# Optimization experiments

Hardware: AMD Instinct MI355X
Metric: run time of the kernel (lower is better)

Reference implementation:

```python
import jax, jax.numpy as jnp
import numpy as np


def setup_inputs() -> dict:
    key = jax.random.key(0)
    k1, k2, k3 = jax.random.split(key, 3)
    num, c_in, c_out, nx, ny, din, dout = 128, 3, 8, 31, 31, 4, 6
    x = jax.random.normal(k1, (num, c_in, din, nx + 1, ny + 1), dtype=jnp.float32)
    tensors = jax.random.normal(k2, (c_in, c_out, nx, ny, din, din, din, din, dout), dtype=jnp.float32)
    bias = jax.random.normal(k3, (c_out, nx, ny, dout), dtype=jnp.float32) * 1e-8
    return {"x": x, "tensors": tensors, "bias": bias}


def reference(x, tensors, bias):
    # x: [num, c_in, din, sx, sy]; tensors: [c_in, c_out, nx, ny, din,din,din,din, dout]
    num, c_in, din, sx, sy = x.shape
    X, Y = sx - 1, sy - 1  # == nx, ny
    c_out, dout = tensors.shape[1], tensors.shape[-1]
    # four 2x2-patch corners, each [num, c_in, din, X, Y]
    a = x[:, :, :, :-1, :-1]
    b = x[:, :, :, 1:, :-1]
    c = x[:, :, :, :-1, 1:]
    d = x[:, :, :, 1:, 1:]
    # outer product of the four corner vectors -> rank-4 local feature [num, c_in, din^4, X, Y]
    ab = jnp.einsum('ncixy,ncjxy->ncijxy', a, b)
    cd = jnp.einsum('nckxy,nclxy->ncklxy', c, d)
    patch = jnp.einsum('ncijxy,ncklxy->ncijklxy', ab, cd)
    patch = patch.reshape(num, c_in, din ** 4, X, Y)
    # per-position weight: [c_in, c_out, X, Y, din^4, dout]
    w = tensors.reshape(c_in, c_out, X, Y, din ** 4, dout)
    out = jnp.einsum('ncmxy,cpxymo->npoxy', patch, w)  # [num, c_out, dout, X, Y]
    out = out + bias.transpose(0, 3, 1, 2)[None]  # bias -> [1, c_out, dout, X, Y]
    return out
```

## Files before the change

kernel.cpp:

```cpp
#include <hip/hip_runtime.h>
#include <hip/hip_bf16.h>


typedef __attribute__((ext_vector_type(8))) short short8;
typedef __attribute__((ext_vector_type(4))) float floatx4;

#define WS_ELEMS (961u * 6144u)
#define SW_STR 72

static __device__ __forceinline__ unsigned pkbf(float lo, float hi) {
  __hip_bfloat162 h = __float22bfloat162_rn(make_float2(lo, hi));
  union { __hip_bfloat162 h; unsigned u; } v;
  v.h = h;
  return v.u;
}

template <bool TO_WS>
__global__ __launch_bounds__(256, 4)
void ttn_conv_mfma(const float* __restrict__ x,
                   const float* __restrict__ tensors,
                   const float* __restrict__ bias,
                   float* __restrict__ dst) {
  __shared__ __align__(16) unsigned short sW[2][48 * SW_STR];

  const int site = blockIdx.x;
  const int xx = site / 31, yy = site - xx * 31;
  const int t = threadIdx.x;
  const int lane = t & 63, wave = t >> 6;
  const int row = lane & 15, quad = lane >> 4;

  const int p_st = t >> 5, q_st = t & 31;

  floatx4 acc[2][3];
#pragma unroll
  for (int i0 = 0; i0 < 2; ++i0)
#pragma unroll
    for (int j0 = 0; j0 < 3; ++j0)
      acc[i0][j0] = (floatx4){0.f, 0.f, 0.f, 0.f};

  float a4[2][4], b2[2][2], cd8[2][8];
  float4 wv0, wv1, wv2;

  auto loadW = [&](int c, int mb) {
    const float* src = tensors +
        ((size_t)((c * 8 + p_st) * 961 + site)) * 1536 + (size_t)(mb * 64 + 2 * q_st) * 6;
    wv0 = *(const float4*)src;
    wv1 = *(const float4*)(src + 4);
    wv2 = *(const float4*)(src + 8);
  };
  auto storeW = [&](int buf) {
    const float vv[12] = {wv0.x, wv0.y, wv0.z, wv0.w, wv1.x, wv1.y,
                          wv1.z, wv1.w, wv2.x, wv2.y, wv2.z, wv2.w};
#pragma unroll
    for (int o = 0; o < 6; ++o)
      *(unsigned*)&sW[buf][(p_st * 6 + o) * SW_STR + 2 * q_st] = pkbf(vv[o], vv[o + 6]);
  };
  auto loadFactors = [&](int c) {
#pragma unroll
    for (int mt = 0; mt < 2; ++mt) {
      const int n = wave * 32 + mt * 16 + row;
      const float* xb = x + ((size_t)n * 3 + c) * 4096 + xx * 32 + yy;
      float dq[4];
#pragma unroll
      for (int i = 0; i < 4; ++i) {
        a4[mt][i] = xb[i * 1024];
        dq[i]     = xb[i * 1024 + 33];
      }
      b2[mt][0] = xb[(quad >> 1) * 1024 + 32];
      b2[mt][1] = xb[(2 + (quad >> 1)) * 1024 + 32];
      const float cq0 = xb[(2 * (quad & 1)) * 1024 + 1];
      const float cq1 = xb[(2 * (quad & 1) + 1) * 1024 + 1];
#pragma unroll
      for (int j = 0; j < 8; ++j)
        cd8[mt][j] = (j < 4 ? cq0 : cq1) * dq[j & 3];
    }
  };

  loadW(0, 0);
  storeW(0);
  loadW(0, 1);
  loadFactors(0);

  for (int c = 0; c < 3; ++c) {
    if (c) loadFactors(c);
#pragma unroll
    for (int mb = 0; mb < 4; ++mb) {
      const int ch = c * 4 + mb;
      const int bp = mb & 1;
      __syncthreads();

#pragma unroll
      for (int ks = 0; ks < 2; ++ks) {
        short8 bfr[3];
#pragma unroll
        for (int nt = 0; nt < 3; ++nt)
          bfr[nt] = *(const short8*)&sW[bp][(nt * 16 + row) * SW_STR + ks * 32 + quad * 8];
#pragma unroll
        for (int mt = 0; mt < 2; ++mt) {
          const float ab = a4[mt][mb] * b2[mt][ks];
          union { unsigned u[4]; short8 s; } af;
#pragma unroll
          for (int jj = 0; jj < 4; ++jj)
            af.u[jj] = pkbf(ab * cd8[mt][2 * jj], ab * cd8[mt][2 * jj + 1]);
#pragma unroll
          for (int nt = 0; nt < 3; ++nt)
            acc[mt][nt] = __builtin_amdgcn_mfma_f32_16x16x32_bf16(
                af.s, bfr[nt], acc[mt][nt], 0, 0, 0);
        }
      }

      if (ch < 11) storeW(1 - bp);
      if (ch < 10) {
        const int i2 = ch + 2;
        loadW(i2 >> 2, i2 & 3);
      }
    }
  }

  if (TO_WS) {
#pragma unroll
    for (int mt = 0; mt < 2; ++mt)
#pragma unroll
      for (int r = 0; r < 4; ++r) {
        const int n = wave * 32 + mt * 16 + quad * 4 + r;
#pragma unroll
        for (int nt = 0; nt < 3; ++nt) {
          const int po = nt * 16 + row;
          dst[(size_t)site * 6144 + n * 48 + po] = acc[mt][nt][r];
        }
      }
  } else {
#pragma unroll
    for (int mt = 0; mt < 2; ++mt)
#pragma unroll
      for (int r = 0; r < 4; ++r) {
        const int n = wave * 32 + mt * 16 + quad * 4 + r;
#pragma unroll
        for (int nt = 0; nt < 3; ++nt) {
          const int po = nt * 16 + row;
          const int p = po / 6, o = po - p * 6;
          dst[(size_t)(n * 48 + po) * 961 + site] =
              acc[mt][nt][r] + bias[(p * 961 + site) * 6 + o];
        }
      }
  }
}

__global__ __launch_bounds__(256, 8)
void ttn_transpose_bias(const float* __restrict__ ws,
                        const float* __restrict__ bias,
                        float* __restrict__ out) {
  __shared__ float tile[32][33];
  const int f0 = blockIdx.x * 32;
  const int s0 = blockIdx.y * 32;
  const int tx = threadIdx.x;
  const int ty = threadIdx.y;

#pragma unroll
  for (int rr = 0; rr < 4; ++rr) {
    const int srow = ty + rr * 8;
    const int site = s0 + srow;
    if (site < 961)
      tile[srow][tx] = ws[(size_t)site * 6144 + f0 + tx];
  }
  __syncthreads();

#pragma unroll
  for (int rr = 0; rr < 4; ++rr) {
    const int fy = ty + rr * 8;
    const int f = f0 + fy;
    const int site = s0 + tx;
    if (site < 961) {
      const int po = f % 48;
      const int p = po / 6, o = po - p * 6;
      out[(size_t)f * 961 + site] = tile[tx][fy] + bias[(p * 961 + site) * 6 + o];
    }
  }
}

extern "C" void kernel_launch(void* const* d_in, const int* in_sizes, int n_in,
                              void* d_out, int out_size, void* d_ws, size_t ws_size,
                              hipStream_t stream) {
  const float* x       = (const float*)d_in[0];
  const float* tensors = (const float*)d_in[1];
  const float* bias    = (const float*)d_in[2];
  float* out           = (float*)d_out;

  const size_t need = (size_t)WS_ELEMS * sizeof(float);
  if (d_ws != nullptr && ws_size >= need) {
    float* ws = (float*)d_ws;
    hipLaunchKernelGGL((ttn_conv_mfma<true>), dim3(961), dim3(256), 0, stream,
                       x, tensors, bias, ws);
    hipLaunchKernelGGL(ttn_transpose_bias, dim3(192, 31), dim3(32, 8), 0, stream,
                       ws, bias, out);
  } else {
    hipLaunchKernelGGL((ttn_conv_mfma<false>), dim3(961), dim3(256), 0, stream,
                       x, tensors, bias, out);
  }
}
```

Baseline: 255.4 us.

## Process two weight chunks per barrier stage and prefetch raw x factors early

The shared-memory weight tile is widened so each double-buffered stage holds two 64-column chunks. That halves the number of __syncthreads across the 12 chunks, and the store and next global load now happen before each stage's MFMAs. The x corner values are fetched with float2 loads one stage ahead of when they are turned into a/b/cd factors, hiding their global latency behind MFMA work. The cost is more live registers (twice the weight prefetch registers plus raw x buffers) under a 4-blocks-per-CU launch bound, which risks spills or lower occupancy. Both a larger LDS footprint and unaligned float2 loads are possible side costs.

```diff
diff --git a/kernel.cpp b/kernel.cpp
--- a/kernel.cpp
+++ b/kernel.cpp
@@ -6,7 +6,7 @@
 typedef __attribute__((ext_vector_type(4))) float floatx4;
 
 #define WS_ELEMS (961u * 6144u)
-#define SW_STR 72
+#define SW_COLS 136
 
 static __device__ __forceinline__ unsigned pkbf(float lo, float hi) {
   __hip_bfloat162 h = __float22bfloat162_rn(make_float2(lo, hi));
@@ -21,7 +21,7 @@
                    const float* __restrict__ tensors,
                    const float* __restrict__ bias,
                    float* __restrict__ dst) {
-  __shared__ __align__(16) unsigned short sW[2][48 * SW_STR];
+  __shared__ __align__(16) unsigned short sW[2][48 * SW_COLS];
 
   const int site = blockIdx.x;
   const int xx = site / 31, yy = site - xx * 31;
@@ -39,82 +39,97 @@
       acc[i0][j0] = (floatx4){0.f, 0.f, 0.f, 0.f};
 
   float a4[2][4], b2[2][2], cd8[2][8];
-  float4 wv0, wv1, wv2;
-
-  auto loadW = [&](int c, int mb) {
-    const float* src = tensors +
-        ((size_t)((c * 8 + p_st) * 961 + site)) * 1536 + (size_t)(mb * 64 + 2 * q_st) * 6;
-    wv0 = *(const float4*)src;
-    wv1 = *(const float4*)(src + 4);
-    wv2 = *(const float4*)(src + 8);
-  };
-  auto storeW = [&](int buf) {
-    const float vv[12] = {wv0.x, wv0.y, wv0.z, wv0.w, wv1.x, wv1.y,
-                          wv1.z, wv1.w, wv2.x, wv2.y, wv2.z, wv2.w};
-#pragma unroll
-    for (int o = 0; o < 6; ++o)
-      *(unsigned*)&sW[buf][(p_st * 6 + o) * SW_STR + 2 * q_st] = pkbf(vv[o], vv[o + 6]);
-  };
-  auto loadFactors = [&](int c) {
+  float2 rAC[2][4], rBD[2][4];
+  float4 wv[6];
+
+  auto loadPair = [&](int s) {
+    const int c = s >> 1;
+    const float* base = tensors + ((size_t)((c * 8 + p_st) * 961 + site)) * 1536;
+#pragma unroll
+    for (int h = 0; h < 2; ++h) {
+      const float* src = base + (size_t)((2 * (s & 1) + h) * 64 + 2 * q_st) * 6;
+      wv[h * 3 + 0] = *(const float4*)src;
+      wv[h * 3 + 1] = *(const float4*)(src + 4);
+      wv[h * 3 + 2] = *(const float4*)(src + 8);
+    }
+  };
+  auto storePair = [&](int buf) {
+#pragma unroll
+    for (int h = 0; h < 2; ++h) {
+      const float4 w0 = wv[h * 3], w1 = wv[h * 3 + 1], w2 = wv[h * 3 + 2];
+      const float vv[12] = {w0.x, w0.y, w0.z, w0.w, w1.x, w1.y,
+                            w1.z, w1.w, w2.x, w2.y, w2.z, w2.w};
+#pragma unroll
+      for (int o = 0; o < 6; ++o)
+        *(unsigned*)&sW[buf][(p_st * 6 + o) * SW_COLS + h * 64 + 2 * q_st] =
+            pkbf(vv[o], vv[o + 6]);
+    }
+  };
+  auto loadRaw = [&](int c) {
 #pragma unroll
     for (int mt = 0; mt < 2; ++mt) {
       const int n = wave * 32 + mt * 16 + row;
       const float* xb = x + ((size_t)n * 3 + c) * 4096 + xx * 32 + yy;
-      float dq[4];
 #pragma unroll
       for (int i = 0; i < 4; ++i) {
-        a4[mt][i] = xb[i * 1024];
-        dq[i]     = xb[i * 1024 + 33];
-      }
-      b2[mt][0] = xb[(quad >> 1) * 1024 + 32];
-      b2[mt][1] = xb[(2 + (quad >> 1)) * 1024 + 32];
-      const float cq0 = xb[(2 * (quad & 1)) * 1024 + 1];
-      const float cq1 = xb[(2 * (quad & 1) + 1) * 1024 + 1];
+        rAC[mt][i] = *(const float2*)(xb + i * 1024);
+        rBD[mt][i] = *(const float2*)(xb + i * 1024 + 32);
+      }
+    }
+  };
+  auto cvtFactors = [&]() {
+    const int qh = quad >> 1, ql = quad & 1;
+#pragma unroll
+    for (int mt = 0; mt < 2; ++mt) {
+#pragma unroll
+      for (int i = 0; i < 4; ++i) a4[mt][i] = rAC[mt][i].x;
+      b2[mt][0] = qh ? rBD[mt][1].x : rBD[mt][0].x;
+      b2[mt][1] = qh ? rBD[mt][3].x : rBD[mt][2].x;
+      const float cq0 = ql ? rAC[mt][2].y : rAC[mt][0].y;
+      const float cq1 = ql ? rAC[mt][3].y : rAC[mt][1].y;
 #pragma unroll
       for (int j = 0; j < 8; ++j)
-        cd8[mt][j] = (j < 4 ? cq0 : cq1) * dq[j & 3];
-    }
-  };
-
-  loadW(0, 0);
-  storeW(0);
-  loadW(0, 1);
-  loadFactors(0);
-
-  for (int c = 0; c < 3; ++c) {
-    if (c) loadFactors(c);
-#pragma unroll
-    for (int mb = 0; mb < 4; ++mb) {
-      const int ch = c * 4 + mb;
-      const int bp = mb & 1;
-      __syncthreads();
-
-#pragma unroll
-      for (int ks = 0; ks < 2; ++ks) {
-        short8 bfr[3];
+        cd8[mt][j] = (j < 4 ? cq0 : cq1) * rBD[mt][j & 3].y;
+    }
+  };
+
+  loadPair(0);
+  loadRaw(0);
+  cvtFactors();
+  storePair(0);
+  loadPair(1);
+  __syncthreads();
+
+#pragma unroll
+  for (int s = 0; s < 6; ++s) {
+    const int bp = s & 1;
+    if (s <= 4) storePair(1 - bp);
+    if (s <= 3) loadPair(s + 2);
+    if (s == 1) loadRaw(1);
+    if (s == 3) loadRaw(2);
+    if (s == 2 || s == 4) cvtFactors();
+
+#pragma unroll
+    for (int ks = 0; ks < 4; ++ks) {
+      const int mb = 2 * (s & 1) + (ks >> 1);
+      short8 bfr[3];
+#pragma unroll
+      for (int nt = 0; nt < 3; ++nt)
+        bfr[nt] = *(const short8*)&sW[bp][(nt * 16 + row) * SW_COLS + ks * 32 + quad * 8];
+#pragma unroll
+      for (int mt = 0; mt < 2; ++mt) {
+        const float ab = a4[mt][mb] * b2[mt][ks & 1];
+        union { unsigned u[4]; short8 s8; } af;
+#pragma unroll
+        for (int jj = 0; jj < 4; ++jj)
+          af.u[jj] = pkbf(ab * cd8[mt][2 * jj], ab * cd8[mt][2 * jj + 1]);
 #pragma unroll
         for (int nt = 0; nt < 3; ++nt)
-          bfr[nt] = *(const short8*)&sW[bp][(nt * 16 + row) * SW_STR + ks * 32 + quad * 8];
-#pragma unroll
-        for (int mt = 0; mt < 2; ++mt) {
-          const float ab = a4[mt][mb] * b2[mt][ks];
-          union { unsigned u[4]; short8 s; } af;
-#pragma unroll
-          for (int jj = 0; jj < 4; ++jj)
-            af.u[jj] = pkbf(ab * cd8[mt][2 * jj], ab * cd8[mt][2 * jj + 1]);
-#pragma unroll
-          for (int nt = 0; nt < 3; ++nt)
-            acc[mt][nt] = __builtin_amdgcn_mfma_f32_16x16x32_bf16(
-                af.s, bfr[nt], acc[mt][nt], 0, 0, 0);
-        }
-      }
-
-      if (ch < 11) storeW(1 - bp);
-      if (ch < 10) {
-        const int i2 = ch + 2;
-        loadW(i2 >> 2, i2 & 3);
-      }
-    }
+          acc[mt][nt] = __builtin_amdgcn_mfma_f32_16x16x32_bf16(
+              af.s8, bfr[nt], acc[mt][nt], 0, 0, 0);
+      }
+    }
+    if (s < 5) __syncthreads();
   }
 
   if (TO_WS) {
```

New measurement: 245.4 us. 3.9% less time.
